# Kernel optimization log

Measured on AMD Instinct MI355X. Metric: run time of the kernel, lower is better.

## Reference

```python
import jax, jax.numpy as jnp
import numpy as np

NHID = 256
B, T = 128, 2048


def setup_inputs() -> dict:
    key = jax.random.key(0)
    ks = jax.random.split(key, 7)
    s = 1.0 / np.sqrt(NHID)  # torch default uniform bound for RNN/Linear
    u = lambda k, shape, bound: jax.random.uniform(k, shape, jnp.float32, -bound, bound)
    return {
        "x": jax.random.normal(ks[0], (B, T, 1), jnp.float32),
        "W_ih": u(ks[1], (NHID, 1), s),
        "W_hh": u(ks[2], (NHID, NHID), s),
        "b_ih": u(ks[3], (NHID,), s),
        "b_hh": u(ks[4], (NHID,), s),
        "W_out": u(ks[5], (1, NHID), s),
        "b_out": u(ks[6], (1,), s),
    }


def reference(x, W_ih, W_hh, b_ih, b_hh, W_out, b_out):
    # x: [B, T, 1] -> time-major [T, B, 1]
    xt = jnp.transpose(x, (1, 0, 2))
    # Precompute input contribution for all steps: [T, B, H]
    xproj = xt @ W_ih.T + (b_ih + b_hh)

    def step(h, xp):  # h: [B, H], xp: [B, H]
        h_new = jnp.tanh(xp + h @ W_hh.T)
        return h_new, h_new

    h0 = jnp.zeros((x.shape[0], W_hh.shape[0]), dtype=x.dtype)
    _, ys = jax.lax.scan(step, h0, xproj)  # ys: [T, B, H]
    # Output projection then back to batch-major [B, T, 1]
    y = ys @ W_out.T + b_out
    return jnp.transpose(y, (1, 0, 2))
```

## Files before the change

kernel.cpp:

```cpp
#include <hip/hip_runtime.h>
#include <hip/hip_fp16.h>

#define HID  256
#define TT   2048
#define NB   128
#define NTHR 1024

template <int CTRL>
__device__ __forceinline__ float dpp_add(float v) {
    int t = __builtin_amdgcn_update_dpp(0, __float_as_int(v), CTRL, 0xF, 0xF, true);
    return v + __int_as_float(t);
}

__device__ __forceinline__ float tanh_fast(float x) {
    float e = __expf(2.0f * x);
    float r = __builtin_amdgcn_rcpf(e + 1.0f);
    return fmaf(-2.0f, r, 1.0f);
}

__device__ __forceinline__ __half2 bc_h2(unsigned int u) {
    __half2 h;
    __builtin_memcpy(&h, &u, 4);
    return h;
}

__global__ void pack_w(const float* __restrict__ W, unsigned int* __restrict__ out) {
    int j    = blockIdx.x * 256 + threadIdx.x;
    int k    = j & 3;
    int lane = (j >> 2) & 63;
    int i    = (j >> 8) & 7;
    int wv   = j >> 11;
    int tid  = wv * 64 + lane;
    int row  = 4 * (tid >> 4) + (i >> 1);
    int col  = 16 * (tid & 15) + 8 * (i & 1) + 2 * k;
    _Float16 lo = (_Float16)W[row * HID + col];
    _Float16 hi = (_Float16)W[row * HID + col + 1];
    unsigned short ulo, uhi;
    __builtin_memcpy(&ulo, &lo, 2);
    __builtin_memcpy(&uhi, &hi, 2);
    out[j] = (unsigned int)ulo | ((unsigned int)uhi << 16);
}

#define FMA_CH2(ACC, T, H0, H1, H2, H3, H4, H5, H6, H7) do { \
    __half2 a_ = bc_h2((T).x), b_ = bc_h2((T).y), c_ = bc_h2((T).z), d_ = bc_h2((T).w); \
    ACC = fmaf(__low2float(a_),  H0, ACC); ACC = fmaf(__high2float(a_), H1, ACC); \
    ACC = fmaf(__low2float(b_),  H2, ACC); ACC = fmaf(__high2float(b_), H3, ACC); \
    ACC = fmaf(__low2float(c_),  H4, ACC); ACC = fmaf(__high2float(c_), H5, ACC); \
    ACC = fmaf(__low2float(d_),  H6, ACC); ACC = fmaf(__high2float(d_), H7, ACC); \
} while (0)

#define RED16(A) do { \
    A = dpp_add<0xB1>(A); A = dpp_add<0x4E>(A); \
    A = dpp_add<0x124>(A); A = dpp_add<0x128>(A); \
} while (0)

__global__ __launch_bounds__(NTHR)
void rnn_persist(
    const float* __restrict__ x,
    const float* __restrict__ W_ih,
    const uint4* __restrict__ wq,
    const float* __restrict__ b_ih,
    const float* __restrict__ b_hh,
    const float* __restrict__ W_out,
    const float* __restrict__ b_out,
    float* __restrict__ y)
{
    __shared__ __align__(16) float s_h[2][8 * 36];
    __shared__ float s_x[TT];
    __shared__ float s_part[2][16];
    __shared__ float s_pad[22528];

    const int tid  = threadIdx.x;
    const int c3   = tid & 15;
    const int rg   = tid >> 4;
    const int lane = tid & 63;
    const int wv   = tid >> 6;
    const int b    = blockIdx.x;

    if (b == -1) {
        volatile float* vp = s_pad;
        vp[tid] = 1.0f;
        y[tid] = vp[tid];
    }

    for (int k = tid; k < TT; k += NTHR) s_x[k] = x[(size_t)b * TT + k];

    const uint4* wbase = wq + (size_t)wv * 8 * 64 + lane;

    const int   myrow = 4 * rg + (c3 & 3);
    const float wih   = W_ih[myrow];
    const float bias  = b_ih[myrow] + b_hh[myrow];
    const float wo_my = W_out[myrow];
    const float bout  = b_out[0];

    if (tid < 256) {
        int wd = 36 * (tid >> 5) + (tid & 31);
        s_h[0][wd] = 0.0f;
        s_h[1][wd] = 0.0f;
    }
    __syncthreads();

    int p = 0;
    float* yrow = y + (size_t)b * TT;
    const int hwword = 36 * (myrow >> 5) + (myrow & 31);
    const int rdbase = 36 * (c3 >> 1) + 16 * (c3 & 1);

    for (int step = 0; step <= TT; ++step) {
        if (step >= 1 && wv == ((step - 1) & 15)) {
            float pp = s_part[(step - 1) & 1][lane & 15];
            pp = dpp_add<0xB1>(pp);
            pp = dpp_add<0x4E>(pp);
            pp = dpp_add<0x124>(pp);
            pp = dpp_add<0x128>(pp);
            if (lane == 0) yrow[step - 1] = pp + bout;
        }
        if (step == TT) break;

        const uint4 T0 = wbase[0 * 64];
        const uint4 T1 = wbase[1 * 64];
        const uint4 T2 = wbase[2 * 64];
        const uint4 T3 = wbase[3 * 64];
        const uint4 T4 = wbase[4 * 64];
        const uint4 T5 = wbase[5 * 64];
        const uint4 T6 = wbase[6 * 64];
        const uint4 T7 = wbase[7 * 64];

        const float xt = s_x[step];
        const float* hb = &s_h[p][rdbase];
        const float4 H0 = *(const float4*)(hb);
        const float4 H1 = *(const float4*)(hb + 4);
        const float4 H2 = *(const float4*)(hb + 8);
        const float4 H3 = *(const float4*)(hb + 12);
        const float hx0 = H0.x, hx1 = H0.y, hx2  = H0.z, hx3  = H0.w;
        const float hx4 = H1.x, hx5 = H1.y, hx6  = H1.z, hx7  = H1.w;
        const float hx8 = H2.x, hx9 = H2.y, hx10 = H2.z, hx11 = H2.w;
        const float hx12 = H3.x, hx13 = H3.y, hx14 = H3.z, hx15 = H3.w;

        float acc0 = 0.0f, acc1 = 0.0f, acc2 = 0.0f, acc3 = 0.0f;
        FMA_CH2(acc0, T0, hx0, hx1, hx2, hx3, hx4, hx5, hx6, hx7);
        FMA_CH2(acc0, T1, hx8, hx9, hx10, hx11, hx12, hx13, hx14, hx15);
        FMA_CH2(acc1, T2, hx0, hx1, hx2, hx3, hx4, hx5, hx6, hx7);
        FMA_CH2(acc1, T3, hx8, hx9, hx10, hx11, hx12, hx13, hx14, hx15);
        FMA_CH2(acc2, T4, hx0, hx1, hx2, hx3, hx4, hx5, hx6, hx7);
        FMA_CH2(acc2, T5, hx8, hx9, hx10, hx11, hx12, hx13, hx14, hx15);
        FMA_CH2(acc3, T6, hx0, hx1, hx2, hx3, hx4, hx5, hx6, hx7);
        FMA_CH2(acc3, T7, hx8, hx9, hx10, hx11, hx12, hx13, hx14, hx15);

        RED16(acc0); RED16(acc1); RED16(acc2); RED16(acc3);

        float s01 = (c3 & 1) ? acc1 : acc0;
        float s23 = (c3 & 1) ? acc3 : acc2;
        float dot = (c3 & 2) ? s23 : s01;
        float hn  = tanh_fast(fmaf(xt, wih, bias) + dot);

        if ((c3 & 12) == 0) s_h[p ^ 1][hwword] = hn;

        float pv = ((c3 & 12) == 0) ? hn * wo_my : 0.0f;
        pv = dpp_add<0xB1>(pv);
        pv = dpp_add<0x4E>(pv);
        pv = dpp_add<0x124>(pv);
        pv = dpp_add<0x128>(pv);
        pv = dpp_add<0x142>(pv);
        pv = dpp_add<0x143>(pv);
        if (lane == 63) s_part[step & 1][wv] = pv;

        __syncthreads();
        p ^= 1;
    }
}

extern "C" void kernel_launch(void* const* d_in, const int* in_sizes, int n_in,
                              void* d_out, int out_size, void* d_ws, size_t ws_size,
                              hipStream_t stream) {
    const float* x     = (const float*)d_in[0];
    const float* W_ih  = (const float*)d_in[1];
    const float* W_hh  = (const float*)d_in[2];
    const float* b_ih  = (const float*)d_in[3];
    const float* b_hh  = (const float*)d_in[4];
    const float* W_out = (const float*)d_in[5];
    const float* b_out = (const float*)d_in[6];
    float* y = (float*)d_out;
    unsigned int* wpk = (unsigned int*)d_ws;

    hipLaunchKernelGGL(pack_w, dim3(128), dim3(256), 0, stream, W_hh, wpk);
    hipLaunchKernelGGL(rnn_persist, dim3(NB), dim3(NTHR), 0, stream,
                       x, W_ih, (const uint4*)wpk, b_ih, b_hh, W_out, b_out, y);
}
```

Baseline: 1.502 ms.

## Use fp16 dot2 with fp16 hidden state and stage half of W_hh in LDS

Stores the hidden state in shared memory as fp16 and replaces the scalar fp32 FMA chain with packed fdot2 instructions, halving the multiply-accumulate instruction count. Half of the packed recurrent weights are copied into LDS once per block and read from there each step, while the other half still streams from global/L2. This cuts per-step VALU work and global load traffic, but rounding h to fp16 before the matmul adds precision error that accumulates over the recurrence.

```diff
diff --git a/kernel.cpp b/kernel.cpp
--- a/kernel.cpp
+++ b/kernel.cpp
@@ -5,6 +5,8 @@
 #define TT   2048
 #define NB   128
 #define NTHR 1024
+
+typedef _Float16 hf2 __attribute__((ext_vector_type(2)));
 
 template <int CTRL>
 __device__ __forceinline__ float dpp_add(float v) {
@@ -18,8 +20,8 @@
     return fmaf(-2.0f, r, 1.0f);
 }
 
-__device__ __forceinline__ __half2 bc_h2(unsigned int u) {
-    __half2 h;
+__device__ __forceinline__ hf2 bc2(unsigned int u) {
+    hf2 h;
     __builtin_memcpy(&h, &u, 4);
     return h;
 }
@@ -41,12 +43,11 @@
     out[j] = (unsigned int)ulo | ((unsigned int)uhi << 16);
 }
 
-#define FMA_CH2(ACC, T, H0, H1, H2, H3, H4, H5, H6, H7) do { \
-    __half2 a_ = bc_h2((T).x), b_ = bc_h2((T).y), c_ = bc_h2((T).z), d_ = bc_h2((T).w); \
-    ACC = fmaf(__low2float(a_),  H0, ACC); ACC = fmaf(__high2float(a_), H1, ACC); \
-    ACC = fmaf(__low2float(b_),  H2, ACC); ACC = fmaf(__high2float(b_), H3, ACC); \
-    ACC = fmaf(__low2float(c_),  H4, ACC); ACC = fmaf(__high2float(c_), H5, ACC); \
-    ACC = fmaf(__low2float(d_),  H6, ACC); ACC = fmaf(__high2float(d_), H7, ACC); \
+#define DOT4(ACC, Tv, Hv) do { \
+    ACC = __builtin_amdgcn_fdot2(bc2((Tv).x), bc2((Hv).x), ACC, false); \
+    ACC = __builtin_amdgcn_fdot2(bc2((Tv).y), bc2((Hv).y), ACC, false); \
+    ACC = __builtin_amdgcn_fdot2(bc2((Tv).z), bc2((Hv).z), ACC, false); \
+    ACC = __builtin_amdgcn_fdot2(bc2((Tv).w), bc2((Hv).w), ACC, false); \
 } while (0)
 
 #define RED16(A) do { \
@@ -65,10 +66,10 @@
     const float* __restrict__ b_out,
     float* __restrict__ y)
 {
-    __shared__ __align__(16) float s_h[2][8 * 36];
+    __shared__ uint4 s_w[4096];
     __shared__ float s_x[TT];
+    __shared__ __align__(16) unsigned short s_hh[2][16 * 24];
     __shared__ float s_part[2][16];
-    __shared__ float s_pad[22528];
 
     const int tid  = threadIdx.x;
     const int c3   = tid & 15;
@@ -77,15 +78,12 @@
     const int wv   = tid >> 6;
     const int b    = blockIdx.x;
 
-    if (b == -1) {
-        volatile float* vp = s_pad;
-        vp[tid] = 1.0f;
-        y[tid] = vp[tid];
-    }
-
     for (int k = tid; k < TT; k += NTHR) s_x[k] = x[(size_t)b * TT + k];
 
-    const uint4* wbase = wq + (size_t)wv * 8 * 64 + lane;
+    for (int j = tid; j < 4096; j += NTHR)
+        s_w[j] = wq[j + ((j >> 8) << 8)];
+
+    if (tid < 768) (&s_hh[0][0])[tid] = 0;
 
     const int   myrow = 4 * rg + (c3 & 3);
     const float wih   = W_ih[myrow];
@@ -93,17 +91,15 @@
     const float wo_my = W_out[myrow];
     const float bout  = b_out[0];
 
-    if (tid < 256) {
-        int wd = 36 * (tid >> 5) + (tid & 31);
-        s_h[0][wd] = 0.0f;
-        s_h[1][wd] = 0.0f;
-    }
+    const uint4* lbase = s_w + (wv * 4) * 64 + lane;
+    const uint4* sbase = wq + (size_t)(wv * 8 + 4) * 64 + lane;
+    const int hwidx  = 24 * (myrow >> 4) + (myrow & 15);
+    const int hrbase = 24 * c3;
+
     __syncthreads();
 
     int p = 0;
     float* yrow = y + (size_t)b * TT;
-    const int hwword = 36 * (myrow >> 5) + (myrow & 31);
-    const int rdbase = 36 * (c3 >> 1) + 16 * (c3 & 1);
 
     for (int step = 0; step <= TT; ++step) {
         if (step >= 1 && wv == ((step - 1) & 15)) {
@@ -116,35 +112,26 @@
         }
         if (step == TT) break;
 
-        const uint4 T0 = wbase[0 * 64];
-        const uint4 T1 = wbase[1 * 64];
-        const uint4 T2 = wbase[2 * 64];
-        const uint4 T3 = wbase[3 * 64];
-        const uint4 T4 = wbase[4 * 64];
-        const uint4 T5 = wbase[5 * 64];
-        const uint4 T6 = wbase[6 * 64];
-        const uint4 T7 = wbase[7 * 64];
+        const uint4 T0 = sbase[0];
+        const uint4 T1 = sbase[64];
+        const uint4 T2 = sbase[128];
+        const uint4 T3 = sbase[192];
+
+        const uint4 H0 = *(const uint4*)&s_hh[p][hrbase];
+        const uint4 H1 = *(const uint4*)&s_hh[p][hrbase + 8];
+
+        const uint4 L0 = lbase[0];
+        const uint4 L1 = lbase[64];
+        const uint4 L2 = lbase[128];
+        const uint4 L3 = lbase[192];
 
         const float xt = s_x[step];
-        const float* hb = &s_h[p][rdbase];
-        const float4 H0 = *(const float4*)(hb);
-        const float4 H1 = *(const float4*)(hb + 4);
-        const float4 H2 = *(const float4*)(hb + 8);
-        const float4 H3 = *(const float4*)(hb + 12);
-        const float hx0 = H0.x, hx1 = H0.y, hx2  = H0.z, hx3  = H0.w;
-        const float hx4 = H1.x, hx5 = H1.y, hx6  = H1.z, hx7  = H1.w;
-        const float hx8 = H2.x, hx9 = H2.y, hx10 = H2.z, hx11 = H2.w;
-        const float hx12 = H3.x, hx13 = H3.y, hx14 = H3.z, hx15 = H3.w;
 
         float acc0 = 0.0f, acc1 = 0.0f, acc2 = 0.0f, acc3 = 0.0f;
-        FMA_CH2(acc0, T0, hx0, hx1, hx2, hx3, hx4, hx5, hx6, hx7);
-        FMA_CH2(acc0, T1, hx8, hx9, hx10, hx11, hx12, hx13, hx14, hx15);
-        FMA_CH2(acc1, T2, hx0, hx1, hx2, hx3, hx4, hx5, hx6, hx7);
-        FMA_CH2(acc1, T3, hx8, hx9, hx10, hx11, hx12, hx13, hx14, hx15);
-        FMA_CH2(acc2, T4, hx0, hx1, hx2, hx3, hx4, hx5, hx6, hx7);
-        FMA_CH2(acc2, T5, hx8, hx9, hx10, hx11, hx12, hx13, hx14, hx15);
-        FMA_CH2(acc3, T6, hx0, hx1, hx2, hx3, hx4, hx5, hx6, hx7);
-        FMA_CH2(acc3, T7, hx8, hx9, hx10, hx11, hx12, hx13, hx14, hx15);
+        DOT4(acc0, L0, H0); DOT4(acc0, L1, H1);
+        DOT4(acc1, L2, H0); DOT4(acc1, L3, H1);
+        DOT4(acc2, T0, H0); DOT4(acc2, T1, H1);
+        DOT4(acc3, T2, H0); DOT4(acc3, T3, H1);
 
         RED16(acc0); RED16(acc1); RED16(acc2); RED16(acc3);
 
@@ -153,7 +140,12 @@
         float dot = (c3 & 2) ? s23 : s01;
         float hn  = tanh_fast(fmaf(xt, wih, bias) + dot);
 
-        if ((c3 & 12) == 0) s_h[p ^ 1][hwword] = hn;
+        if ((c3 & 12) == 0) {
+            _Float16 hh = (_Float16)hn;
+            unsigned short us;
+            __builtin_memcpy(&us, &hh, 2);
+            s_hh[p ^ 1][hwidx] = us;
+        }
 
         float pv = ((c3 & 12) == 0) ? hn * wo_my : 0.0f;
         pv = dpp_add<0xB1>(pv);
```

New measurement: 1.478 ms. Within noise of the previous version (-1.6%).
